# Kernel optimization log

Hardware: AMD Instinct MI355X
Metric: run time of the kernel (lower is better)

Reference implementation:

```python
import jax, jax.numpy as jnp
import numpy as np

ORIENTATIONS = 8
CELL = 16          # pixels_per_cell = (16, 16)
EPS = 1e-5         # skimage L2-Hys eps


def _hog_features(x):
    """x: [B, H, W, C] float image. Faithful to skimage.feature.hog with
    orientations=8, pixels_per_cell=(16,16), cells_per_block=(1,1),
    block_norm='L2-Hys', multichannel gradient selection."""
    B, H, W, C = x.shape
    # per-channel central-difference gradients, zero at borders (skimage _hog_channel_gradient)
    g_row = jnp.zeros_like(x).at[:, 1:-1, :, :].set(x[:, 2:, :, :] - x[:, :-2, :, :])
    g_col = jnp.zeros_like(x).at[:, :, 1:-1, :].set(x[:, :, 2:, :] - x[:, :, :-2, :])
    magn_ch = jnp.hypot(g_row, g_col)                      # [B,H,W,C]
    # pick channel with max gradient magnitude per pixel
    idx = jnp.argmax(magn_ch, axis=-1, keepdims=True)      # [B,H,W,1]
    gr = jnp.take_along_axis(g_row, idx, axis=-1)[..., 0]  # [B,H,W]
    gc = jnp.take_along_axis(g_col, idx, axis=-1)[..., 0]
    magn = jnp.take_along_axis(magn_ch, idx, axis=-1)[..., 0]
    # orientation in degrees, mod 180 (unsigned gradients)
    ori = jnp.degrees(jnp.arctan2(gr, gc)) % 180.0
    bin_width = 180.0 / ORIENTATIONS
    bin_idx = jnp.clip(jnp.floor(ori / bin_width).astype(jnp.int32), 0, ORIENTATIONS - 1)
    ncr, ncc = H // CELL, W // CELL
    # per-cell mean magnitude for each orientation bin
    hists = []
    for o in range(ORIENTATIONS):
        m = jnp.where(bin_idx == o, magn, 0.0)             # [B,H,W]
        m = m.reshape(B, ncr, CELL, ncc, CELL).mean(axis=(2, 4))  # [B,ncr,ncc]
        hists.append(m)
    hist = jnp.stack(hists, axis=-1)                       # [B,ncr,ncc,O]
    # block normalization: 1x1 cells per block, 'L2-Hys'
    n = hist / jnp.sqrt(jnp.sum(hist * hist, axis=-1, keepdims=True) + EPS ** 2)
    n = jnp.minimum(n, 0.2)
    n = n / jnp.sqrt(jnp.sum(n * n, axis=-1, keepdims=True) + EPS ** 2)
    return n.reshape(B, -1)                                # [B, ncr*ncc*O]


def setup_inputs() -> dict:
    key = jax.random.key(0)
    fake = jax.random.uniform(key, (64, 3, 512, 512), dtype=jnp.float32)
    return {"fake": fake}


def reference(fake) -> jnp.ndarray:
    x = jnp.transpose(fake, (0, 2, 3, 1))  # NCHW -> NHWC (module's permute)
    return _hog_features(x)
```

## Files before the change

### kernel.cpp

```cpp
#include <hip/hip_runtime.h>
#include <math.h>


namespace {

constexpr int Hh = 512;
constexpr int Ww = 512;
constexpr int CHN = 3;
constexpr int HW = Hh * Ww;
constexpr float TAN22 = 0.41421356237309503f;

__device__ __forceinline__ void load_row(const float* __restrict__ xb,
                                         int h, int lane, float dst[CHN][8]) {
    const int hl = h < 0 ? 0 : (h > Hh - 1 ? Hh - 1 : h);
#pragma unroll
    for (int ch = 0; ch < CHN; ++ch) {
        const float4* p =
            (const float4*)(xb + (size_t)ch * HW + (size_t)hl * Ww) + (lane << 1);
        const float4 a = p[0];
        const float4 b = p[1];
        dst[ch][0] = a.x; dst[ch][1] = a.y; dst[ch][2] = a.z; dst[ch][3] = a.w;
        dst[ch][4] = b.x; dst[ch][5] = b.y; dst[ch][6] = b.z; dst[ch][7] = b.w;
    }
}

__global__ __launch_bounds__(256) void hog_kernel(const float* __restrict__ x,
                                                  float* __restrict__ out) {
    const int b     = blockIdx.x >> 4;
    const int band2 = blockIdx.x & 15;
    const int tx    = threadIdx.x;
    const int lane  = tx & 63;
    const int rg    = tx >> 6;
    const int r0    = band2 * 32 + rg * 8;
    const bool isL0  = (lane == 0);
    const bool isL63 = (lane == 63);

    const float* xb = x + (size_t)b * (CHN * HW);

    float c[8];
#pragma unroll
    for (int o = 0; o < 8; ++o) c[o] = 0.f;

    float win[3][CHN][8];
    load_row(xb, r0 - 1, lane, win[0]);
    load_row(xb, r0,     lane, win[1]);
    load_row(xb, r0 + 1, lane, win[2]);

#pragma unroll
    for (int hh = 0; hh < 8; ++hh) {
        const int h = r0 + hh;
        float (*prev)[8] = win[hh % 3];
        float (*cur)[8]  = win[(hh + 1) % 3];
        float (*next)[8] = win[(hh + 2) % 3];
        const bool rowEdge = (h == 0) | (h == Hh - 1);

        float grow[CHN][8];
#pragma unroll
        for (int ch = 0; ch < CHN; ++ch)
#pragma unroll
            for (int i = 0; i < 8; ++i)
                grow[ch][i] = rowEdge ? 0.f : next[ch][i] - prev[ch][i];

        if (hh < 7) load_row(xb, h + 2, lane, win[hh % 3]);

        float shL[CHN], shR[CHN];
#pragma unroll
        for (int ch = 0; ch < CHN; ++ch) {
            shL[ch] = __shfl_up(cur[ch][7], 1, 64);
            shR[ch] = __shfl_down(cur[ch][0], 1, 64);
        }

#pragma unroll
        for (int i = 0; i < 8; ++i) {
            float bm2 = -1.f, bgr = 0.f, bgc = 0.f;
#pragma unroll
            for (int ch = 0; ch < CHN; ++ch) {
                const float gl = (i == 0) ? shL[ch] : cur[ch][i - 1];
                const float gr_ = (i == 7) ? shR[ch] : cur[ch][i + 1];
                float gcol = gr_ - gl;
                if (i == 0) gcol = isL0 ? 0.f : gcol;
                if (i == 7) gcol = isL63 ? 0.f : gcol;
                const float gv = grow[ch][i];
                const float m2 = fmaf(gv, gv, gcol * gcol);
                if (m2 > bm2) { bm2 = m2; bgr = gv; bgc = gcol; }
            }
            const float m = sqrtf(bm2);

            const bool flip = (bgr < 0.f) | ((bgr == 0.f) & (bgc < 0.f));
            const float bb = flip ? -bgr : bgr;
            const float A  = flip ? -bgc : bgc;
            const float Aa = fabsf(A);
            const float p1 = Aa * TAN22;
            const float p2 = bb * TAN22;
            const bool q2  = (A <= 0.f);
            const bool ge1 = (bb >= p1), ge2 = (bb >= Aa), ge3 = (p2 >= Aa);
            const bool gt1 = (bb > p1),  gt2 = (bb > Aa),  gt3 = (p2 > Aa);
            c[0] += m;
            c[1] += (q2 | ge1) ? m : 0.f;
            c[2] += (q2 | ge2) ? m : 0.f;
            c[3] += (q2 | ge3) ? m : 0.f;
            c[4] += q2 ? m : 0.f;
            c[5] += (q2 & !gt3) ? m : 0.f;
            c[6] += (q2 & !gt2) ? m : 0.f;
            c[7] += (q2 & !gt1) ? m : 0.f;
        }
    }

#pragma unroll
    for (int o = 0; o < 8; ++o) c[o] += __shfl_xor(c[o], 1, 64);

    __shared__ float lhist[4][32][9];
    if (tx < 128) lhist[tx >> 5][tx & 31][8] = 0.f;
    if ((lane & 1) == 0) {
        const int cellc = lane >> 1;
#pragma unroll
        for (int o = 0; o < 8; ++o) lhist[rg][cellc][o] = c[o];
    }
    __syncthreads();

    const int cell = tx >> 3;
    const int o    = tx & 7;
#pragma unroll
    for (int band = 0; band < 2; ++band) {
        const float c_o  = lhist[2 * band][cell][o]     + lhist[2 * band + 1][cell][o];
        const float c_o1 = lhist[2 * band][cell][o + 1] + lhist[2 * band + 1][cell][o + 1];
        const float hv = (c_o - c_o1) * (1.0f / 256.0f);

        float ss = hv * hv;
        ss += __shfl_xor(ss, 1, 64);
        ss += __shfl_xor(ss, 2, 64);
        ss += __shfl_xor(ss, 4, 64);
        float n1 = hv / sqrtf(ss + 1e-10f);
        n1 = fminf(n1, 0.2f);
        float s2 = n1 * n1;
        s2 += __shfl_xor(s2, 1, 64);
        s2 += __shfl_xor(s2, 2, 64);
        s2 += __shfl_xor(s2, 4, 64);
        const float nv = n1 / sqrtf(s2 + 1e-10f);

        const size_t oi =
            (((size_t)b * 32 + (band2 * 2 + band)) * 32 + cell) * 8 + o;
        out[oi] = nv;
    }
}

}

extern "C" void kernel_launch(void* const* d_in, const int* in_sizes, int n_in,
                              void* d_out, int out_size, void* d_ws, size_t ws_size,
                              hipStream_t stream) {
    (void)n_in; (void)out_size; (void)d_ws; (void)ws_size;
    const float* x = (const float*)d_in[0];
    float* out = (float*)d_out;
    const int B = in_sizes[0] / (CHN * HW);
    const int grid = B * 16;
    hog_kernel<<<grid, 256, 0, stream>>>(x, out);
}
```

Before: 281.5 us.

## Split each block into column halves with 4 pixels per lane and double the grid

```diff
diff --git a/kernel.cpp b/kernel.cpp
--- a/kernel.cpp
+++ b/kernel.cpp
@@ -10,77 +10,92 @@
 constexpr int HW = Hh * Ww;
 constexpr float TAN22 = 0.41421356237309503f;
 
-__device__ __forceinline__ void load_row(const float* __restrict__ xb,
-                                         int h, int lane, float dst[CHN][8]) {
+__device__ __forceinline__ void load_row4(const float* __restrict__ xb,
+                                          int h, int c0, int lane,
+                                          float dst[CHN][4]) {
     const int hl = h < 0 ? 0 : (h > Hh - 1 ? Hh - 1 : h);
 #pragma unroll
     for (int ch = 0; ch < CHN; ++ch) {
-        const float4* p =
-            (const float4*)(xb + (size_t)ch * HW + (size_t)hl * Ww) + (lane << 1);
-        const float4 a = p[0];
-        const float4 b = p[1];
-        dst[ch][0] = a.x; dst[ch][1] = a.y; dst[ch][2] = a.z; dst[ch][3] = a.w;
-        dst[ch][4] = b.x; dst[ch][5] = b.y; dst[ch][6] = b.z; dst[ch][7] = b.w;
+        const float4 v = *(const float4*)(xb + (size_t)ch * HW +
+                                          (size_t)hl * Ww + c0 + (lane << 2));
+        dst[ch][0] = v.x; dst[ch][1] = v.y; dst[ch][2] = v.z; dst[ch][3] = v.w;
     }
 }
 
 __global__ __launch_bounds__(256) void hog_kernel(const float* __restrict__ x,
                                                   float* __restrict__ out) {
-    const int b     = blockIdx.x >> 4;
-    const int band2 = blockIdx.x & 15;
-    const int tx    = threadIdx.x;
-    const int lane  = tx & 63;
-    const int rg    = tx >> 6;
-    const int r0    = band2 * 32 + rg * 8;
-    const bool isL0  = (lane == 0);
-    const bool isL63 = (lane == 63);
+    const int b       = blockIdx.x >> 5;
+    const int cellrow = blockIdx.x & 31;
+    const int tx      = threadIdx.x;
+    const int lane    = tx & 63;
+    const int wid     = tx >> 6;
+    const int colhalf = wid & 1;
+    const int strip   = wid >> 1;
+    const int r0      = cellrow * 16 + strip * 8;
+    const int c0      = colhalf << 8;
 
     const float* xb = x + (size_t)b * (CHN * HW);
+
+    const bool bL = (colhalf == 0) & (lane == 0);
+    const bool bR = (colhalf == 1) & (lane == 63);
+    const int hLoff = (colhalf == 0) ? 0 : 255;
+    const int hRoff = (colhalf == 0) ? 256 : 511;
+
+    float P[CHN][4], C[CHN][4], N[CHN][4], T[CHN][4];
+    load_row4(xb, r0 - 1, c0, lane, P);
+    load_row4(xb, r0,     c0, lane, C);
+    load_row4(xb, r0 + 1, c0, lane, N);
+
+    float hLc[CHN], hRc[CHN], hLn[CHN], hRn[CHN];
+#pragma unroll
+    for (int ch = 0; ch < CHN; ++ch) {
+        const float* rp = xb + (size_t)ch * HW + (size_t)r0 * Ww;
+        hLc[ch] = rp[hLoff];
+        hRc[ch] = rp[hRoff];
+    }
 
     float c[8];
 #pragma unroll
     for (int o = 0; o < 8; ++o) c[o] = 0.f;
 
-    float win[3][CHN][8];
-    load_row(xb, r0 - 1, lane, win[0]);
-    load_row(xb, r0,     lane, win[1]);
-    load_row(xb, r0 + 1, lane, win[2]);
-
-#pragma unroll
+#pragma unroll 1
     for (int hh = 0; hh < 8; ++hh) {
         const int h = r0 + hh;
-        float (*prev)[8] = win[hh % 3];
-        float (*cur)[8]  = win[(hh + 1) % 3];
-        float (*next)[8] = win[(hh + 2) % 3];
+
+        if (hh < 7) load_row4(xb, h + 2, c0, lane, T);
+        {
+            const int hn = (h + 1 > Hh - 1) ? Hh - 1 : h + 1;
+#pragma unroll
+            for (int ch = 0; ch < CHN; ++ch) {
+                const float* rp = xb + (size_t)ch * HW + (size_t)hn * Ww;
+                hLn[ch] = rp[hLoff];
+                hRn[ch] = rp[hRoff];
+            }
+        }
+
         const bool rowEdge = (h == 0) | (h == Hh - 1);
 
-        float grow[CHN][8];
-#pragma unroll
-        for (int ch = 0; ch < CHN; ++ch)
-#pragma unroll
-            for (int i = 0; i < 8; ++i)
-                grow[ch][i] = rowEdge ? 0.f : next[ch][i] - prev[ch][i];
-
-        if (hh < 7) load_row(xb, h + 2, lane, win[hh % 3]);
-
-        float shL[CHN], shR[CHN];
+        float gL[CHN], gR[CHN];
 #pragma unroll
         for (int ch = 0; ch < CHN; ++ch) {
-            shL[ch] = __shfl_up(cur[ch][7], 1, 64);
-            shR[ch] = __shfl_down(cur[ch][0], 1, 64);
+            const float su = __shfl_up(C[ch][3], 1, 64);
+            const float sd = __shfl_down(C[ch][0], 1, 64);
+            gL[ch] = (lane == 0)  ? hLc[ch] : su;
+            gR[ch] = (lane == 63) ? hRc[ch] : sd;
         }
 
 #pragma unroll
-        for (int i = 0; i < 8; ++i) {
+        for (int i = 0; i < 4; ++i) {
             float bm2 = -1.f, bgr = 0.f, bgc = 0.f;
 #pragma unroll
             for (int ch = 0; ch < CHN; ++ch) {
-                const float gl = (i == 0) ? shL[ch] : cur[ch][i - 1];
-                const float gr_ = (i == 7) ? shR[ch] : cur[ch][i + 1];
+                const float gl  = (i == 0) ? gL[ch] : C[ch][i - 1];
+                const float gr_ = (i == 3) ? gR[ch] : C[ch][i + 1];
                 float gcol = gr_ - gl;
-                if (i == 0) gcol = isL0 ? 0.f : gcol;
-                if (i == 7) gcol = isL63 ? 0.f : gcol;
-                const float gv = grow[ch][i];
+                if (i == 0) gcol = bL ? 0.f : gcol;
+                if (i == 3) gcol = bR ? 0.f : gcol;
+                float gv = N[ch][i] - P[ch][i];
+                gv = rowEdge ? 0.f : gv;
                 const float m2 = fmaf(gv, gv, gcol * gcol);
                 if (m2 > bm2) { bm2 = m2; bgr = gv; bgc = gcol; }
             }
@@ -104,44 +119,56 @@
             c[6] += (q2 & !gt2) ? m : 0.f;
             c[7] += (q2 & !gt1) ? m : 0.f;
         }
+
+        if (hh < 7) {
+#pragma unroll
+            for (int ch = 0; ch < CHN; ++ch) {
+#pragma unroll
+                for (int i = 0; i < 4; ++i) {
+                    P[ch][i] = C[ch][i];
+                    C[ch][i] = N[ch][i];
+                    N[ch][i] = T[ch][i];
+                }
+                hLc[ch] = hLn[ch];
+                hRc[ch] = hRn[ch];
+            }
+        }
     }
 
 #pragma unroll
-    for (int o = 0; o < 8; ++o) c[o] += __shfl_xor(c[o], 1, 64);
+    for (int o = 0; o < 8; ++o) {
+        c[o] += __shfl_xor(c[o], 1, 64);
+        c[o] += __shfl_xor(c[o], 2, 64);
+    }
 
-    __shared__ float lhist[4][32][9];
-    if (tx < 128) lhist[tx >> 5][tx & 31][8] = 0.f;
-    if ((lane & 1) == 0) {
-        const int cellc = lane >> 1;
+    __shared__ float lh[2][32][9];
+    if (tx < 64) lh[tx >> 5][tx & 31][8] = 0.f;
+    if ((lane & 3) == 0) {
+        const int cell = (colhalf << 4) + (lane >> 2);
 #pragma unroll
-        for (int o = 0; o < 8; ++o) lhist[rg][cellc][o] = c[o];
+        for (int o = 0; o < 8; ++o) lh[strip][cell][o] = c[o];
     }
     __syncthreads();
 
     const int cell = tx >> 3;
     const int o    = tx & 7;
-#pragma unroll
-    for (int band = 0; band < 2; ++band) {
-        const float c_o  = lhist[2 * band][cell][o]     + lhist[2 * band + 1][cell][o];
-        const float c_o1 = lhist[2 * band][cell][o + 1] + lhist[2 * band + 1][cell][o + 1];
-        const float hv = (c_o - c_o1) * (1.0f / 256.0f);
+    const float c_o  = lh[0][cell][o]     + lh[1][cell][o];
+    const float c_o1 = lh[0][cell][o + 1] + lh[1][cell][o + 1];
+    const float hv = (c_o - c_o1) * (1.0f / 256.0f);
 
-        float ss = hv * hv;
-        ss += __shfl_xor(ss, 1, 64);
-        ss += __shfl_xor(ss, 2, 64);
-        ss += __shfl_xor(ss, 4, 64);
-        float n1 = hv / sqrtf(ss + 1e-10f);
-        n1 = fminf(n1, 0.2f);
-        float s2 = n1 * n1;
-        s2 += __shfl_xor(s2, 1, 64);
-        s2 += __shfl_xor(s2, 2, 64);
-        s2 += __shfl_xor(s2, 4, 64);
-        const float nv = n1 / sqrtf(s2 + 1e-10f);
+    float ss = hv * hv;
+    ss += __shfl_xor(ss, 1, 64);
+    ss += __shfl_xor(ss, 2, 64);
+    ss += __shfl_xor(ss, 4, 64);
+    float n1 = hv / sqrtf(ss + 1e-10f);
+    n1 = fminf(n1, 0.2f);
+    float s2 = n1 * n1;
+    s2 += __shfl_xor(s2, 1, 64);
+    s2 += __shfl_xor(s2, 2, 64);
+    s2 += __shfl_xor(s2, 4, 64);
+    const float nv = n1 / sqrtf(s2 + 1e-10f);
 
-        const size_t oi =
-            (((size_t)b * 32 + (band2 * 2 + band)) * 32 + cell) * 8 + o;
-        out[oi] = nv;
-    }
+    out[(((size_t)b * 32 + cellrow) * 32 + cell) * 8 + o] = nv;
 }
 
 }
@@ -153,6 +180,6 @@
     const float* x = (const float*)d_in[0];
     float* out = (float*)d_out;
     const int B = in_sizes[0] / (CHN * HW);
-    const int grid = B * 16;
+    const int grid = B * 32;
     hog_kernel<<<grid, 256, 0, stream>>>(x, out);
 }
```

New measurement: 282.9 us. About the same (+0.5%).
